# Optimization experiments

Measured on AMD Instinct MI355X. Metric: run time of the kernel, lower is better.

## Reference

```python
import jax, jax.numpy as jnp
import numpy as np

N = 100000      # nodes
E = 3200000     # edges
F_IN = 9        # atom features
H = 128         # hidden_dim
L = 4           # num_layers
G = 512         # graphs in batch
BN_EPS = 1e-5


def setup_inputs() -> dict:
    key = jax.random.key(0)
    ks = jax.random.split(key, 24)
    s = 0.05
    inp = {}
    inp["x"] = jax.random.normal(ks[0], (N, F_IN), jnp.float32)
    inp["edge_index"] = jax.random.randint(ks[1], (2, E), 0, N, dtype=jnp.int64)
    inp["batch"] = jnp.sort(jax.random.randint(ks[2], (N,), 0, G, dtype=jnp.int64))
    # atom embedding
    inp["Wemb"] = jax.random.normal(ks[3], (F_IN, H), jnp.float32) * s
    inp["bemb"] = jnp.zeros((H,), jnp.float32)
    # per-layer GINConv params (stacked over L layers)
    inp["eps"] = jnp.zeros((L,), jnp.float32)  # train_eps=True, init 0
    inp["W1"] = jax.random.normal(ks[4], (L, H, 2 * H), jnp.float32) * s
    inp["b1"] = jnp.zeros((L, 2 * H), jnp.float32)
    inp["g1"] = jax.random.uniform(ks[5], (L, 2 * H), jnp.float32, 0.9, 1.1)
    inp["be1"] = jax.random.normal(ks[6], (L, 2 * H), jnp.float32) * s
    inp["m1"] = jax.random.normal(ks[7], (L, 2 * H), jnp.float32) * s
    inp["v1"] = jax.random.uniform(ks[8], (L, 2 * H), jnp.float32, 0.5, 1.5)
    inp["W2"] = jax.random.normal(ks[9], (L, 2 * H, H), jnp.float32) * s
    inp["b2"] = jnp.zeros((L, H), jnp.float32)
    # outer BatchNorm per layer
    inp["g2"] = jax.random.uniform(ks[10], (L, H), jnp.float32, 0.9, 1.1)
    inp["be2"] = jax.random.normal(ks[11], (L, H), jnp.float32) * s
    inp["m2"] = jax.random.normal(ks[12], (L, H), jnp.float32) * s
    inp["v2"] = jax.random.uniform(ks[13], (L, H), jnp.float32, 0.5, 1.5)
    return inp


def _bn(x, g, b, m, v):
    # eval-mode BatchNorm1d with running stats
    return g * (x - m) * jax.lax.rsqrt(v + BN_EPS) + b


def reference(x, edge_index, batch, Wemb, bemb, eps, W1, b1, g1, be1, m1, v1,
              W2, b2, g2, be2, m2, v2):
    h = x @ Wemb + bemb                                   # [N, H]
    src, dst = edge_index[0], edge_index[1]
    for i in range(L):
        # GIN aggregation: sum of neighbor (source) features into target
        agg = jax.ops.segment_sum(h[src], dst, num_segments=N)   # [N, H]
        z = (1.0 + eps[i]) * h + agg
        # MLP: Linear -> BN -> ReLU -> Linear
        z = jax.nn.relu(_bn(z @ W1[i] + b1[i], g1[i], be1[i], m1[i], v1[i]))
        h = z @ W2[i] + b2[i]
        # outer BN + ReLU (dropout skipped: eval mode)
        h = jax.nn.relu(_bn(h, g2[i], be2[i], m2[i], v2[i]))
    # global_mean_pool
    sums = jax.ops.segment_sum(h, batch, num_segments=G)          # [G, H]
    counts = jax.ops.segment_sum(jnp.ones((N, 1), h.dtype), batch,
                                 num_segments=G)                  # [G, 1]
    return sums / jnp.maximum(counts, 1.0)
```

## Files before the change

### kernel.cpp

```cpp
#include <hip/hip_runtime.h>
#include <stdint.h>

#define H 128
#define H2 256
#define NLAYERS 4
#define BN_EPS 1e-5f

#define BSHIFT 10
#define NPB 1024
#define NBC 98
#define PART_BATCH 2048
#define EPT 8

typedef __attribute__((ext_vector_type(4))) float f32x4;
typedef __attribute__((ext_vector_type(8))) short bhalf8;

__device__ __forceinline__ float bf2f(unsigned short u) {
    union { unsigned int i; float f; } v;
    v.i = ((unsigned int)u) << 16;
    return v.f;
}
__device__ __forceinline__ unsigned short f2bf(float f) {
    union { float f; unsigned int i; } v;
    v.f = f;
    unsigned int b = v.i + 0x7FFFu + ((v.i >> 16) & 1u);
    return (unsigned short)(b >> 16);
}

__global__ __launch_bounds__(256) void embed_kernel(
    const float* __restrict__ x, const float* __restrict__ Wemb,
    const float* __restrict__ bemb, unsigned short* __restrict__ h, int N) {
    int n = blockIdx.x * 2 + (threadIdx.x >> 7);
    int f = threadIdx.x & 127;
    if (n >= N) return;
    const float* xr = x + (size_t)n * 9;
    float acc = bemb[f];
#pragma unroll
    for (int k = 0; k < 9; k++) acc += xr[k] * Wemb[k * H + f];
    h[(size_t)n * H + f] = f2bf(acc);
}

__global__ void prep_params(
    const float* __restrict__ b1, const float* __restrict__ g1, const float* __restrict__ be1,
    const float* __restrict__ m1, const float* __restrict__ v1,
    const float* __restrict__ b2, const float* __restrict__ g2, const float* __restrict__ be2,
    const float* __restrict__ m2, const float* __restrict__ v2,
    float* __restrict__ sc1, float* __restrict__ sh1,
    float* __restrict__ sc2, float* __restrict__ sh2) {
    int t = threadIdx.x;
    if (t < NLAYERS * H2) {
        float s = g1[t] * rsqrtf(v1[t] + BN_EPS);
        sc1[t] = s;
        sh1[t] = (b1[t] - m1[t]) * s + be1[t];
    }
    if (t < NLAYERS * H) {
        float s = g2[t] * rsqrtf(v2[t] + BN_EPS);
        sc2[t] = s;
        sh2[t] = (b2[t] - m2[t]) * s + be2[t];
    }
}

__global__ __launch_bounds__(256) void prep_weights(
    const float* __restrict__ W1, const float* __restrict__ W2,
    unsigned short* __restrict__ W1T, unsigned short* __restrict__ W2T) {
    int idx = blockIdx.x * 256 + threadIdx.x;
    if (idx >= NLAYERS * H * H2) return;
    int l = idx >> 15;
    {
        int r = idx & 32767;
        int c = r >> 7, k = r & 127;
        W1T[idx] = f2bf(W1[((size_t)l * H + k) * H2 + c]);
    }
    {
        int r = idx & 32767;
        int c = r >> 8, k = r & 255;
        W2T[idx] = f2bf(W2[((size_t)l * H2 + k) * H + c]);
    }
}

__global__ __launch_bounds__(256) void hist_coarse(const int* __restrict__ ei,
                                                   unsigned* __restrict__ bc_cnt,
                                                   int E, int nbc) {
    __shared__ unsigned lh[NBC];
    for (int i = threadIdx.x; i < nbc; i += 256) lh[i] = 0;
    __syncthreads();
    for (int e = blockIdx.x * 256 + threadIdx.x; e < E; e += gridDim.x * 256)
        atomicAdd(&lh[(unsigned)ei[E + e] >> BSHIFT], 1u);
    __syncthreads();
    for (int i = threadIdx.x; i < nbc; i += 256)
        if (lh[i]) atomicAdd(&bc_cnt[i], lh[i]);
}

__global__ __launch_bounds__(128) void scan_coarse(const unsigned* __restrict__ bc_cnt,
                                                   unsigned* __restrict__ bc_base,
                                                   unsigned* __restrict__ bc_cursor,
                                                   int nbc, int E) {
    __shared__ unsigned sd[128];
    int t = threadIdx.x;
    unsigned v = (t < nbc) ? bc_cnt[t] : 0u;
    sd[t] = v;
    __syncthreads();
    for (int off = 1; off < 128; off <<= 1) {
        unsigned xv = (t >= off) ? sd[t - off] : 0u;
        __syncthreads();
        sd[t] += xv;
        __syncthreads();
    }
    unsigned excl = sd[t] - v;
    if (t < nbc) {
        bc_base[t] = excl;
        bc_cursor[t] = excl;
    }
    if (t == 0) bc_base[nbc] = (unsigned)E;
}

__global__ __launch_bounds__(256) void partition_kernel(const int* __restrict__ ei,
                                                        unsigned* __restrict__ bc_cursor,
                                                        uint2* __restrict__ part,
                                                        int E, int nbc) {
    __shared__ unsigned lh[NBC];
    __shared__ unsigned lb[NBC];
    for (int i = threadIdx.x; i < nbc; i += 256) lh[i] = 0;
    __syncthreads();
    int base = blockIdx.x * PART_BATCH;
    int s[EPT], d[EPT];
    unsigned rank[EPT];
    int bk[EPT];
#pragma unroll
    for (int k = 0; k < EPT; k++) {
        int e = base + k * 256 + threadIdx.x;
        if (e < E) {
            s[k] = ei[e];
            d[k] = ei[E + e];
            bk[k] = (unsigned)d[k] >> BSHIFT;
            rank[k] = atomicAdd(&lh[bk[k]], 1u);
        } else bk[k] = -1;
    }
    __syncthreads();
    for (int i = threadIdx.x; i < nbc; i += 256)
        lb[i] = lh[i] ? atomicAdd(&bc_cursor[i], lh[i]) : 0u;
    __syncthreads();
#pragma unroll
    for (int k = 0; k < EPT; k++) {
        if (bk[k] >= 0) {
            unsigned p = lb[bk[k]] + rank[k];
            part[p] = make_uint2((unsigned)s[k], (unsigned)d[k]);
        }
    }
}

__global__ __launch_bounds__(1024) void bucket_degrees(const uint2* __restrict__ part,
                                                       const unsigned* __restrict__ bc_base,
                                                       unsigned* __restrict__ gdeg, int N) {
    __shared__ unsigned deg[NPB];
    int b = blockIdx.x;
    deg[threadIdx.x] = 0;
    __syncthreads();
    unsigned r0 = bc_base[b], r1 = bc_base[b + 1];
    for (unsigned i = r0 + threadIdx.x; i < r1; i += 1024)
        atomicAdd(&deg[part[i].y & (NPB - 1)], 1u);
    __syncthreads();
    int node = (b << BSHIFT) + threadIdx.x;
    if (node < N) gdeg[node] = deg[threadIdx.x];
}

__global__ __launch_bounds__(256) void scanA_kernel(const unsigned* __restrict__ deg,
                                                    unsigned* __restrict__ rowptr,
                                                    unsigned* __restrict__ bsum, int N) {
    __shared__ unsigned sd[256];
    int tid = threadIdx.x;
    int base = blockIdx.x * 1024 + tid * 4;
    unsigned v[4];
    unsigned s = 0;
#pragma unroll
    for (int j = 0; j < 4; j++) {
        v[j] = (base + j < N) ? deg[base + j] : 0u;
        s += v[j];
    }
    sd[tid] = s;
    __syncthreads();
    for (int off = 1; off < 256; off <<= 1) {
        unsigned xv = (tid >= off) ? sd[tid - off] : 0u;
        __syncthreads();
        sd[tid] += xv;
        __syncthreads();
    }
    unsigned excl = sd[tid] - s;
#pragma unroll
    for (int j = 0; j < 4; j++) {
        if (base + j < N) rowptr[base + j] = excl;
        excl += v[j];
    }
    if (tid == 255) bsum[blockIdx.x] = sd[255];
}

__global__ __launch_bounds__(1024) void scanB_kernel(unsigned* __restrict__ bsum, int nb) {
    __shared__ unsigned sd[1024];
    int t = threadIdx.x;
    unsigned s = (t < nb) ? bsum[t] : 0u;
    sd[t] = s;
    __syncthreads();
    for (int off = 1; off < 1024; off <<= 1) {
        unsigned xv = (t >= off) ? sd[t - off] : 0u;
        __syncthreads();
        sd[t] += xv;
        __syncthreads();
    }
    if (t < nb) bsum[t] = sd[t] - s;
}

__global__ __launch_bounds__(256) void scanC_kernel(unsigned* __restrict__ rowptr,
                                                    const unsigned* __restrict__ bsum,
                                                    int N, int E) {
    int base = blockIdx.x * 1024 + threadIdx.x * 4;
    unsigned off = bsum[blockIdx.x];
#pragma unroll
    for (int j = 0; j < 4; j++) {
        int i = base + j;
        if (i < N) rowptr[i] += off;
    }
    if (blockIdx.x == 0 && threadIdx.x == 0) rowptr[N] = (unsigned)E;
}

__global__ __launch_bounds__(1024) void bucket_fill(const uint2* __restrict__ part,
                                                    const unsigned* __restrict__ bc_base,
                                                    const unsigned* __restrict__ rowptr,
                                                    unsigned* __restrict__ col, int N) {
    __shared__ unsigned cur[NPB];
    int b = blockIdx.x;
    int node = (b << BSHIFT) + threadIdx.x;
    cur[threadIdx.x] = (node < N) ? rowptr[node] : 0u;
    __syncthreads();
    unsigned r0 = bc_base[b], r1 = bc_base[b + 1];
    for (unsigned i = r0 + threadIdx.x; i < r1; i += 1024) {
        uint2 e = part[i];
        unsigned p = atomicAdd(&cur[e.y & (NPB - 1)], 1u);
        col[p] = e.x;
    }
}

__global__ __launch_bounds__(128) void agg_kernel(
    const unsigned short* __restrict__ h, const unsigned* __restrict__ rowptr,
    const unsigned* __restrict__ col, const float* __restrict__ eps, int layer,
    unsigned short* __restrict__ z, int N) {
    int n = blockIdx.x * 2 + (threadIdx.x >> 6);
    if (n >= N) return;
    int lane = threadIdx.x & 63;
    int chunk = lane & 15;
    int sub = lane >> 4;
    unsigned r0 = rowptr[n], r1 = rowptr[n + 1];
    float acc0[8], acc1[8];
#pragma unroll
    for (int k = 0; k < 8; k++) { acc0[k] = 0.f; acc1[k] = 0.f; }
    unsigned j = r0 + sub;
    for (; j + 4 < r1; j += 8) {
        unsigned c0 = col[j], c1 = col[j + 4];
        bhalf8 v0 = *(const bhalf8*)&h[(size_t)c0 * H + chunk * 8];
        bhalf8 v1 = *(const bhalf8*)&h[(size_t)c1 * H + chunk * 8];
#pragma unroll
        for (int k = 0; k < 8; k++) {
            acc0[k] += bf2f((unsigned short)v0[k]);
            acc1[k] += bf2f((unsigned short)v1[k]);
        }
    }
    if (j < r1) {
        unsigned c0 = col[j];
        bhalf8 v0 = *(const bhalf8*)&h[(size_t)c0 * H + chunk * 8];
#pragma unroll
        for (int k = 0; k < 8; k++) acc0[k] += bf2f((unsigned short)v0[k]);
    }
#pragma unroll
    for (int k = 0; k < 8; k++) {
        acc0[k] += acc1[k];
        acc0[k] += __shfl_xor(acc0[k], 16, 64);
        acc0[k] += __shfl_xor(acc0[k], 32, 64);
    }
    if (sub == 0) {
        float e = 1.0f + eps[layer];
        bhalf8 hv = *(const bhalf8*)&h[(size_t)n * H + chunk * 8];
        bhalf8 o;
#pragma unroll
        for (int k = 0; k < 8; k++)
            o[k] = (short)f2bf(e * bf2f((unsigned short)hv[k]) + acc0[k]);
        *(bhalf8*)&z[(size_t)n * H + chunk * 8] = o;
    }
}

#define LDP 264
__global__ __launch_bounds__(256) void mlp_fused_kernel(
    const unsigned short* __restrict__ z, const unsigned short* __restrict__ W1T,
    const unsigned short* __restrict__ W2T,
    const float* __restrict__ sc1, const float* __restrict__ sh1,
    const float* __restrict__ sc2, const float* __restrict__ sh2,
    unsigned short* __restrict__ h, int N) {
    __shared__ unsigned short tl[64 * LDP];
    int wave = threadIdx.x >> 6, lane = threadIdx.x & 63;
    int rtile = blockIdx.x * 64;
    int rlane = lane & 15;
    int kq = lane >> 4;
    int kg = kq * 8;
    int arow[4];
#pragma unroll
    for (int rb = 0; rb < 4; rb++) {
        int r = rtile + rb * 16 + rlane;
        arow[rb] = r < N ? r : N - 1;
    }
    f32x4 zero = {0.f, 0.f, 0.f, 0.f};
    {
        int wcol = wave * 64;
        f32x4 acc[4][4];
#pragma unroll
        for (int rb = 0; rb < 4; rb++)
#pragma unroll
            for (int cb = 0; cb < 4; cb++) acc[rb][cb] = zero;
#pragma unroll
        for (int ks = 0; ks < 4; ks++) {
            bhalf8 a[4], b[4];
#pragma unroll
            for (int rb = 0; rb < 4; rb++)
                a[rb] = *(const bhalf8*)&z[(size_t)arow[rb] * H + ks * 32 + kg];
#pragma unroll
            for (int cb = 0; cb < 4; cb++)
                b[cb] = *(const bhalf8*)&W1T[(size_t)(wcol + cb * 16 + rlane) * H + ks * 32 + kg];
#pragma unroll
            for (int rb = 0; rb < 4; rb++)
#pragma unroll
                for (int cb = 0; cb < 4; cb++)
                    acc[rb][cb] = __builtin_amdgcn_mfma_f32_16x16x32_bf16(a[rb], b[cb], acc[rb][cb], 0, 0, 0);
        }
#pragma unroll
        for (int cb = 0; cb < 4; cb++) {
            int colc = wcol + cb * 16 + rlane;
            float sc = sc1[colc], sh = sh1[colc];
#pragma unroll
            for (int rb = 0; rb < 4; rb++) {
#pragma unroll
                for (int j = 0; j < 4; j++) {
                    int rl = rb * 16 + kq * 4 + j;
                    float vv = acc[rb][cb][j] * sc + sh;
                    vv = vv > 0.f ? vv : 0.f;
                    tl[rl * LDP + colc] = f2bf(vv);
                }
            }
        }
    }
    __syncthreads();
    {
        int wcol = wave * 32;
        f32x4 acc[4][2];
#pragma unroll
        for (int rb = 0; rb < 4; rb++)
#pragma unroll
            for (int cb = 0; cb < 2; cb++) acc[rb][cb] = zero;
#pragma unroll
        for (int ks = 0; ks < 8; ks++) {
            bhalf8 a[4], b[2];
#pragma unroll
            for (int rb = 0; rb < 4; rb++)
                a[rb] = *(const bhalf8*)&tl[(rb * 16 + rlane) * LDP + ks * 32 + kg];
#pragma unroll
            for (int cb = 0; cb < 2; cb++)
                b[cb] = *(const bhalf8*)&W2T[(size_t)(wcol + cb * 16 + rlane) * H2 + ks * 32 + kg];
#pragma unroll
            for (int rb = 0; rb < 4; rb++)
#pragma unroll
                for (int cb = 0; cb < 2; cb++)
                    acc[rb][cb] = __builtin_amdgcn_mfma_f32_16x16x32_bf16(a[rb], b[cb], acc[rb][cb], 0, 0, 0);
        }
        int rr = rtile + kq * 4;
#pragma unroll
        for (int cb = 0; cb < 2; cb++) {
            int colc = wcol + cb * 16 + rlane;
            float sc = sc2[colc], sh = sh2[colc];
#pragma unroll
            for (int rb = 0; rb < 4; rb++) {
#pragma unroll
                for (int j = 0; j < 4; j++) {
                    int row = rr + rb * 16 + j;
                    if (row < N) {
                        float vv = acc[rb][cb][j] * sc + sh;
                        vv = vv > 0.f ? vv : 0.f;
                        h[(size_t)row * H + colc] = f2bf(vv);
                    }
                }
            }
        }
    }
}

__global__ __launch_bounds__(128) void pool_kernel(
    const unsigned short* __restrict__ h, const int* __restrict__ batch,
    float* __restrict__ out, int N, int G) {
    __shared__ int se[2];
    int g = blockIdx.x;
    if (threadIdx.x == 0) {
        int lo = 0, hi = N;
        while (lo < hi) {
            int mid = (lo + hi) >> 1;
            if (batch[mid] < g) lo = mid + 1; else hi = mid;
        }
        se[0] = lo;
        hi = N;
        while (lo < hi) {
            int mid = (lo + hi) >> 1;
            if (batch[mid] < g + 1) lo = mid + 1; else hi = mid;
        }
        se[1] = lo;
    }
    __syncthreads();
    int s = se[0], e = se[1];
    int f = threadIdx.x;
    float acc = 0.f;
    for (int r = s; r < e; ++r) acc += bf2f(h[(size_t)r * H + f]);
    int cnt = e - s;
    out[(size_t)g * H + f] = cnt > 0 ? acc / (float)cnt : 0.f;
}

extern "C" void kernel_launch(void* const* d_in, const int* in_sizes, int n_in,
                              void* d_out, int out_size, void* d_ws, size_t ws_size,
                              hipStream_t stream) {
    const float* x     = (const float*)d_in[0];
    const int*   ei    = (const int*)d_in[1];
    const int*   batch = (const int*)d_in[2];
    const float* Wemb  = (const float*)d_in[3];
    const float* bemb  = (const float*)d_in[4];
    const float* eps   = (const float*)d_in[5];
    const float* W1    = (const float*)d_in[6];
    const float* b1    = (const float*)d_in[7];
    const float* g1    = (const float*)d_in[8];
    const float* be1   = (const float*)d_in[9];
    const float* m1    = (const float*)d_in[10];
    const float* v1    = (const float*)d_in[11];
    const float* W2    = (const float*)d_in[12];
    const float* b2    = (const float*)d_in[13];
    const float* g2    = (const float*)d_in[14];
    const float* be2   = (const float*)d_in[15];
    const float* m2    = (const float*)d_in[16];
    const float* v2    = (const float*)d_in[17];

    int N = in_sizes[0] / 9;
    int E = in_sizes[1] / 2;
    int G = out_size / H;
    int nbc = (N + NPB - 1) >> BSHIFT;

    char* p = (char*)d_ws;
    auto alloc = [&](size_t bytes) -> char* {
        char* r = p;
        p += (bytes + 255) & ~(size_t)255;
        return r;
    };
    unsigned short* h   = (unsigned short*)alloc((size_t)N * H * 2);
    unsigned short* z   = (unsigned short*)alloc((size_t)N * H * 2);
    uint2*          part = (uint2*)alloc((size_t)E * 8);
    unsigned*       rowptr = (unsigned*)alloc((size_t)(N + 1) * 4);
    unsigned*       gdeg   = (unsigned*)alloc((size_t)N * 4);
    unsigned*       bsum   = (unsigned*)alloc(1024 * 4);
    unsigned*       col    = (unsigned*)alloc((size_t)E * 4);
    unsigned short* W1T = (unsigned short*)alloc((size_t)NLAYERS * H * H2 * 2);
    unsigned short* W2T = (unsigned short*)alloc((size_t)NLAYERS * H * H2 * 2);
    float* sc1 = (float*)alloc(NLAYERS * H2 * 4);
    float* sh1 = (float*)alloc(NLAYERS * H2 * 4);
    float* sc2 = (float*)alloc(NLAYERS * H * 4);
    float* sh2 = (float*)alloc(NLAYERS * H * 4);
    unsigned* bc_cnt    = (unsigned*)alloc((NBC + 2) * 4);
    unsigned* bc_base   = (unsigned*)alloc((NBC + 2) * 4);
    unsigned* bc_cursor = (unsigned*)alloc((NBC + 2) * 4);

    hipMemsetAsync(bc_cnt, 0, (NBC + 2) * 4, stream);
    prep_params<<<1, 1024, 0, stream>>>(b1, g1, be1, m1, v1, b2, g2, be2, m2, v2,
                                        sc1, sh1, sc2, sh2);
    prep_weights<<<(NLAYERS * H * H2 + 255) / 256, 256, 0, stream>>>(W1, W2, W1T, W2T);
    embed_kernel<<<(N + 1) / 2, 256, 0, stream>>>(x, Wemb, bemb, h, N);

    hist_coarse<<<512, 256, 0, stream>>>(ei, bc_cnt, E, nbc);
    scan_coarse<<<1, 128, 0, stream>>>(bc_cnt, bc_base, bc_cursor, nbc, E);
    partition_kernel<<<(E + PART_BATCH - 1) / PART_BATCH, 256, 0, stream>>>(
        ei, bc_cursor, part, E, nbc);
    bucket_degrees<<<nbc, 1024, 0, stream>>>(part, bc_base, gdeg, N);
    int nb = (N + 1023) / 1024;
    scanA_kernel<<<nb, 256, 0, stream>>>(gdeg, rowptr, bsum, N);
    scanB_kernel<<<1, 1024, 0, stream>>>(bsum, nb);
    scanC_kernel<<<nb, 256, 0, stream>>>(rowptr, bsum, N, E);
    bucket_fill<<<nbc, 1024, 0, stream>>>(part, bc_base, rowptr, col, N);

    for (int l = 0; l < NLAYERS; l++) {
        agg_kernel<<<(N + 1) / 2, 128, 0, stream>>>(h, rowptr, col, eps, l, z, N);
        mlp_fused_kernel<<<(N + 63) / 64, 256, 0, stream>>>(
            z, W1T + (size_t)l * H * H2, W2T + (size_t)l * H * H2,
            sc1 + l * H2, sh1 + l * H2, sc2 + l * H, sh2 + l * H, h, N);
    }
    pool_kernel<<<G, 128, 0, stream>>>(h, batch, (float*)d_out, N, G);
}
```

Measured before the change: 965.1 us.

## Unroll neighbor gather to four loads and pre-swizzle weights into MFMA fragment order

The aggregation kernel now issues four independent neighbor-row loads per iteration with four accumulator sets, and packs four nodes per 256-thread block. This is meant to raise memory-level parallelism on the latency-bound gather. Separately, the weights are pre-permuted into MFMA fragment layout so each lane's B operand is one contiguous coalesced 16-byte load instead of a strided row read. The cost is more registers in the aggregation loop, which may lower occupancy.

```diff
diff --git a/kernel.cpp b/kernel.cpp
--- a/kernel.cpp
+++ b/kernel.cpp
@@ -62,19 +62,28 @@
 
 __global__ __launch_bounds__(256) void prep_weights(
     const float* __restrict__ W1, const float* __restrict__ W2,
-    unsigned short* __restrict__ W1T, unsigned short* __restrict__ W2T) {
+    unsigned short* __restrict__ W1F, unsigned short* __restrict__ W2F) {
     int idx = blockIdx.x * 256 + threadIdx.x;
     if (idx >= NLAYERS * H * H2) return;
-    int l = idx >> 15;
     {
-        int r = idx & 32767;
-        int c = r >> 7, k = r & 127;
-        W1T[idx] = f2bf(W1[((size_t)l * H + k) * H2 + c]);
+        int e = idx & 7;
+        int lane = (idx >> 3) & 63;
+        int ks = (idx >> 9) & 3;
+        int c16 = (idx >> 11) & 15;
+        int l = idx >> 15;
+        int c = c16 * 16 + (lane & 15);
+        int k = ks * 32 + (lane >> 4) * 8 + e;
+        W1F[idx] = f2bf(W1[((size_t)l * H + k) * H2 + c]);
     }
     {
-        int r = idx & 32767;
-        int c = r >> 8, k = r & 255;
-        W2T[idx] = f2bf(W2[((size_t)l * H2 + k) * H + c]);
+        int e = idx & 7;
+        int lane = (idx >> 3) & 63;
+        int ks = (idx >> 9) & 7;
+        int c16 = (idx >> 12) & 7;
+        int l = idx >> 15;
+        int c = c16 * 16 + (lane & 15);
+        int k = ks * 32 + (lane >> 4) * 8 + e;
+        W2F[idx] = f2bf(W2[((size_t)l * H2 + k) * H + c]);
     }
 }
 
@@ -239,41 +248,45 @@
     }
 }
 
-__global__ __launch_bounds__(128) void agg_kernel(
+__global__ __launch_bounds__(256) void agg_kernel(
     const unsigned short* __restrict__ h, const unsigned* __restrict__ rowptr,
     const unsigned* __restrict__ col, const float* __restrict__ eps, int layer,
     unsigned short* __restrict__ z, int N) {
-    int n = blockIdx.x * 2 + (threadIdx.x >> 6);
+    int n = blockIdx.x * 4 + (threadIdx.x >> 6);
     if (n >= N) return;
     int lane = threadIdx.x & 63;
     int chunk = lane & 15;
     int sub = lane >> 4;
     unsigned r0 = rowptr[n], r1 = rowptr[n + 1];
-    float acc0[8], acc1[8];
-#pragma unroll
-    for (int k = 0; k < 8; k++) { acc0[k] = 0.f; acc1[k] = 0.f; }
+    float a0[8], a1[8], a2[8], a3[8];
+#pragma unroll
+    for (int k = 0; k < 8; k++) { a0[k] = 0.f; a1[k] = 0.f; a2[k] = 0.f; a3[k] = 0.f; }
     unsigned j = r0 + sub;
-    for (; j + 4 < r1; j += 8) {
-        unsigned c0 = col[j], c1 = col[j + 4];
+    for (; j + 12 < r1; j += 16) {
+        unsigned c0 = col[j], c1 = col[j + 4], c2 = col[j + 8], c3 = col[j + 12];
         bhalf8 v0 = *(const bhalf8*)&h[(size_t)c0 * H + chunk * 8];
         bhalf8 v1 = *(const bhalf8*)&h[(size_t)c1 * H + chunk * 8];
+        bhalf8 v2 = *(const bhalf8*)&h[(size_t)c2 * H + chunk * 8];
+        bhalf8 v3 = *(const bhalf8*)&h[(size_t)c3 * H + chunk * 8];
 #pragma unroll
         for (int k = 0; k < 8; k++) {
-            acc0[k] += bf2f((unsigned short)v0[k]);
-            acc1[k] += bf2f((unsigned short)v1[k]);
-        }
-    }
-    if (j < r1) {
+            a0[k] += bf2f((unsigned short)v0[k]);
+            a1[k] += bf2f((unsigned short)v1[k]);
+            a2[k] += bf2f((unsigned short)v2[k]);
+            a3[k] += bf2f((unsigned short)v3[k]);
+        }
+    }
+    for (; j < r1; j += 4) {
         unsigned c0 = col[j];
         bhalf8 v0 = *(const bhalf8*)&h[(size_t)c0 * H + chunk * 8];
 #pragma unroll
-        for (int k = 0; k < 8; k++) acc0[k] += bf2f((unsigned short)v0[k]);
+        for (int k = 0; k < 8; k++) a0[k] += bf2f((unsigned short)v0[k]);
     }
 #pragma unroll
     for (int k = 0; k < 8; k++) {
-        acc0[k] += acc1[k];
-        acc0[k] += __shfl_xor(acc0[k], 16, 64);
-        acc0[k] += __shfl_xor(acc0[k], 32, 64);
+        a0[k] += a1[k] + (a2[k] + a3[k]);
+        a0[k] += __shfl_xor(a0[k], 16, 64);
+        a0[k] += __shfl_xor(a0[k], 32, 64);
     }
     if (sub == 0) {
         float e = 1.0f + eps[layer];
@@ -281,15 +294,15 @@
         bhalf8 o;
 #pragma unroll
         for (int k = 0; k < 8; k++)
-            o[k] = (short)f2bf(e * bf2f((unsigned short)hv[k]) + acc0[k]);
+            o[k] = (short)f2bf(e * bf2f((unsigned short)hv[k]) + a0[k]);
         *(bhalf8*)&z[(size_t)n * H + chunk * 8] = o;
     }
 }
 
 #define LDP 264
 __global__ __launch_bounds__(256) void mlp_fused_kernel(
-    const unsigned short* __restrict__ z, const unsigned short* __restrict__ W1T,
-    const unsigned short* __restrict__ W2T,
+    const unsigned short* __restrict__ z, const unsigned short* __restrict__ W1F,
+    const unsigned short* __restrict__ W2F,
     const float* __restrict__ sc1, const float* __restrict__ sh1,
     const float* __restrict__ sc2, const float* __restrict__ sh2,
     unsigned short* __restrict__ h, int N) {
@@ -307,7 +320,6 @@
     }
     f32x4 zero = {0.f, 0.f, 0.f, 0.f};
     {
-        int wcol = wave * 64;
         f32x4 acc[4][4];
 #pragma unroll
         for (int rb = 0; rb < 4; rb++)
@@ -321,7 +333,7 @@
                 a[rb] = *(const bhalf8*)&z[(size_t)arow[rb] * H + ks * 32 + kg];
 #pragma unroll
             for (int cb = 0; cb < 4; cb++)
-                b[cb] = *(const bhalf8*)&W1T[(size_t)(wcol + cb * 16 + rlane) * H + ks * 32 + kg];
+                b[cb] = *(const bhalf8*)&W1F[((size_t)((wave * 4 + cb) * 4 + ks) * 64 + lane) * 8];
 #pragma unroll
             for (int rb = 0; rb < 4; rb++)
 #pragma unroll
@@ -330,7 +342,7 @@
         }
 #pragma unroll
         for (int cb = 0; cb < 4; cb++) {
-            int colc = wcol + cb * 16 + rlane;
+            int colc = wave * 64 + cb * 16 + rlane;
             float sc = sc1[colc], sh = sh1[colc];
 #pragma unroll
             for (int rb = 0; rb < 4; rb++) {
@@ -346,7 +358,6 @@
     }
     __syncthreads();
     {
-        int wcol = wave * 32;
         f32x4 acc[4][2];
 #pragma unroll
         for (int rb = 0; rb < 4; rb++)
@@ -360,7 +371,7 @@
                 a[rb] = *(const bhalf8*)&tl[(rb * 16 + rlane) * LDP + ks * 32 + kg];
 #pragma unroll
             for (int cb = 0; cb < 2; cb++)
-                b[cb] = *(const bhalf8*)&W2T[(size_t)(wcol + cb * 16 + rlane) * H2 + ks * 32 + kg];
+                b[cb] = *(const bhalf8*)&W2F[((size_t)((wave * 2 + cb) * 8 + ks) * 64 + lane) * 8];
 #pragma unroll
             for (int rb = 0; rb < 4; rb++)
 #pragma unroll
@@ -370,7 +381,7 @@
         int rr = rtile + kq * 4;
 #pragma unroll
         for (int cb = 0; cb < 2; cb++) {
-            int colc = wcol + cb * 16 + rlane;
+            int colc = wave * 32 + cb * 16 + rlane;
             float sc = sc2[colc], sh = sh2[colc];
 #pragma unroll
             for (int rb = 0; rb < 4; rb++) {
@@ -456,8 +467,8 @@
     unsigned*       gdeg   = (unsigned*)alloc((size_t)N * 4);
     unsigned*       bsum   = (unsigned*)alloc(1024 * 4);
     unsigned*       col    = (unsigned*)alloc((size_t)E * 4);
-    unsigned short* W1T = (unsigned short*)alloc((size_t)NLAYERS * H * H2 * 2);
-    unsigned short* W2T = (unsigned short*)alloc((size_t)NLAYERS * H * H2 * 2);
+    unsigned short* W1F = (unsigned short*)alloc((size_t)NLAYERS * H * H2 * 2);
+    unsigned short* W2F = (unsigned short*)alloc((size_t)NLAYERS * H * H2 * 2);
     float* sc1 = (float*)alloc(NLAYERS * H2 * 4);
     float* sh1 = (float*)alloc(NLAYERS * H2 * 4);
     float* sc2 = (float*)alloc(NLAYERS * H * 4);
@@ -469,7 +480,7 @@
     hipMemsetAsync(bc_cnt, 0, (NBC + 2) * 4, stream);
     prep_params<<<1, 1024, 0, stream>>>(b1, g1, be1, m1, v1, b2, g2, be2, m2, v2,
                                         sc1, sh1, sc2, sh2);
-    prep_weights<<<(NLAYERS * H * H2 + 255) / 256, 256, 0, stream>>>(W1, W2, W1T, W2T);
+    prep_weights<<<(NLAYERS * H * H2 + 255) / 256, 256, 0, stream>>>(W1, W2, W1F, W2F);
     embed_kernel<<<(N + 1) / 2, 256, 0, stream>>>(x, Wemb, bemb, h, N);
 
     hist_coarse<<<512, 256, 0, stream>>>(ei, bc_cnt, E, nbc);
@@ -484,9 +495,9 @@
     bucket_fill<<<nbc, 1024, 0, stream>>>(part, bc_base, rowptr, col, N);
 
     for (int l = 0; l < NLAYERS; l++) {
-        agg_kernel<<<(N + 1) / 2, 128, 0, stream>>>(h, rowptr, col, eps, l, z, N);
+        agg_kernel<<<(N + 3) / 4, 256, 0, stream>>>(h, rowptr, col, eps, l, z, N);
         mlp_fused_kernel<<<(N + 63) / 64, 256, 0, stream>>>(
-            z, W1T + (size_t)l * H * H2, W2T + (size_t)l * H * H2,
+            z, W1F + (size_t)l * H * H2, W2F + (size_t)l * H * H2,
             sc1 + l * H2, sh1 + l * H2, sc2 + l * H, sh2 + l * H, h, N);
     }
     pool_kernel<<<G, 128, 0, stream>>>(h, batch, (float*)d_out, N, G);
```

Result: faster. 929.2 us (-3.7%).
